# Performance work log

Hardware: AMD Instinct MI355X
Metric: run time of the kernel (lower is better)

## Reference

```python
import jax, jax.numpy as jnp
import numpy as np

BEAM = 8
MAX_LEN = 64
SOS_ID = 1
EOS_ID = 2
NEG = -1e30


def setup_inputs() -> dict:
    key = jax.random.key(0)
    ks = jax.random.split(key, 12)
    B, L, H, V, E = 16, 64, 1024, 32000, 1024
    s = 0.02
    return {
        "dec_hidden": jax.random.normal(ks[0], (B, H), jnp.float32),
        "q_enc_outputs": jax.random.normal(ks[1], (B, L, H), jnp.float32),
        "q_inputs_length": jax.random.randint(ks[2], (B,), 1, L + 1),
        "embedding": jax.random.normal(ks[3], (V, E), jnp.float32) * s,
        "W_ih": jax.random.normal(ks[4], (E, 3 * H), jnp.float32) * s,
        "W_hh": jax.random.normal(ks[5], (H, 3 * H), jnp.float32) * s,
        "b_ih": jnp.zeros((3 * H,), jnp.float32),
        "b_hh": jnp.zeros((3 * H,), jnp.float32),
        "W_c": jax.random.normal(ks[6], (2 * H, H), jnp.float32) * s,
        "W_out": jax.random.normal(ks[7], (H, V), jnp.float32) * s,
        "b_out": jnp.zeros((V,), jnp.float32),
    }


def _beam_search(dec_hidden, q_enc_outputs, q_inputs_length, embedding,
                 W_ih, W_hh, b_ih, b_hh, W_c, W_out, b_out):
    B, H = dec_hidden.shape
    L = q_enc_outputs.shape[1]
    V = W_out.shape[1]
    K = BEAM
    N = B * K
    pos_index = jnp.arange(B)[:, None] * K  # [B,1] offset of each batch's beam block

    # inflate encoder state beam_size times (beam is the inner dim: index = b*K + k)
    hidden = jnp.repeat(dec_hidden, K, axis=0)            # [N,H]
    q_enc = jnp.repeat(q_enc_outputs, K, axis=0)          # [N,L,H]
    q_len = jnp.repeat(q_inputs_length, K, axis=0)        # [N]
    len_mask = jnp.arange(L)[None, :] < q_len[:, None]    # [N,L]

    # only beam 0 of each batch starts live (score 0), rest -inf
    seq_scores = jnp.full((N,), NEG, jnp.float32).at[::K].set(0.0)
    dec_input = jnp.full((N,), SOS_ID, jnp.int32)

    def gru_cell(x, h):
        gx = x @ W_ih + b_ih
        gh = h @ W_hh + b_hh
        xr, xz, xn = jnp.split(gx, 3, axis=-1)
        hr, hz, hn = jnp.split(gh, 3, axis=-1)
        r = jax.nn.sigmoid(xr + hr)
        z = jax.nn.sigmoid(xz + hz)
        n = jnp.tanh(xn + r * hn)
        return (1.0 - z) * n + z * h

    def step(carry, _):
        hidden, seq_scores, dec_input = carry
        x = embedding[dec_input]                               # [N,E]
        h = gru_cell(x, hidden)                                # [N,H]
        # dot-product attention over encoder outputs
        att = jnp.einsum('nh,nlh->nl', h, q_enc) / jnp.sqrt(jnp.float32(H))
        att = jnp.where(len_mask, att, NEG)
        a = jax.nn.softmax(att, axis=-1)
        ctx = jnp.einsum('nl,nlh->nh', a, q_enc)
        o = jnp.tanh(jnp.concatenate([h, ctx], axis=-1) @ W_c)
        logits = o @ W_out + b_out                             # [N,V]
        logp = jax.nn.log_softmax(logits, axis=-1)
        # accumulate scores, flatten beams*vocab per batch, take top-K
        cand = (seq_scores[:, None] + logp).reshape(B, K * V)
        scores, idx = jax.lax.top_k(cand, K)                   # [B,K]
        symbols = (idx % V).reshape(N)
        preds = (idx // V + pos_index).reshape(N)              # predecessor beam rows
        new_hidden = h[preds]
        new_scores = scores.reshape(N)
        stored = new_scores                                     # stored before EOS mask
        new_scores = jnp.where(symbols == EOS_ID, NEG, new_scores)
        return (new_hidden, new_scores, symbols), (stored, preds, symbols)

    _, (all_scores, all_preds, all_syms) = jax.lax.scan(
        step, (hidden, seq_scores, dec_input), None, length=MAX_LEN)

    # backtrack: pick top-K final beams and trace predecessors backwards
    final_scores = all_scores[-1].reshape(B, K)
    sorted_score, sorted_idx = jax.lax.top_k(final_scores, K)
    t_pred = (sorted_idx + pos_index).reshape(N)

    def back(carry, xs):
        syms_t, preds_t = xs
        cur = syms_t[carry]
        return preds_t[carry], cur

    _, seq_rev = jax.lax.scan(back, t_pred, (all_syms[::-1], all_preds[::-1]))
    sequences = seq_rev[::-1].T.reshape(B, BEAM, MAX_LEN)
    return sorted_score, sequences


def reference(dec_hidden, q_enc_outputs, q_inputs_length, embedding,
              W_ih, W_hh, b_ih, b_hh, W_c, W_out, b_out):
    return _beam_search(dec_hidden, q_enc_outputs, q_inputs_length, embedding,
                        W_ih, W_hh, b_ih, b_hh, W_c, W_out, b_out)
```

## Files before the change

kernel.cpp:

```cpp
#include <hip/hip_runtime.h>
#include <cstdint>
#include <cstddef>
#include <climits>

#define Hdim 1024
#define Vdim 32000
#define Lq 64
#define Nrows 128
#define TMAX 64
#define NEGF (-1e30f)

__device__ __forceinline__ bool betterf(float av, int ai, float bv, int bi) {
  return (av > bv) || (av == bv && ai < bi);
}

__device__ __forceinline__ float tanh_xla(float x) {
  float ax = fabsf(x);
  float xc = fminf(fmaxf(x, -7.90531110763549805f), 7.90531110763549805f);
  float x2 = __fmul_rn(xc, xc);
  float p = -2.76076847742355e-16f;
  p = fmaf(p, x2, 2.00018790482477e-13f);
  p = fmaf(p, x2, -8.60467152213735e-11f);
  p = fmaf(p, x2, 5.12229709037114e-08f);
  p = fmaf(p, x2, 1.48572235717979e-05f);
  p = fmaf(p, x2, 6.37261928875436e-04f);
  p = fmaf(p, x2, 4.89352455891786e-03f);
  p = __fmul_rn(xc, p);
  float q = 1.19825839466702e-06f;
  q = fmaf(q, x2, 1.18534705686654e-04f);
  q = fmaf(q, x2, 2.26843463243900e-03f);
  q = fmaf(q, x2, 4.89352518554385e-03f);
  float r = __fdiv_rn(p, q);
  return (ax < 0.0004f) ? x : r;
}

__device__ __forceinline__ float sigmoid_xla(float x) {
  return __fadd_rn(0.5f, __fmul_rn(0.5f, tanh_xla(__fmul_rn(0.5f, x))));
}

__device__ __forceinline__ float exp_xla(float x) {
  x = fminf(x, 88.3762626647950f);
  x = fmaxf(x, -88.3762626647949f);
  float m = floorf(fmaf(x, 1.44269504088896341f, 0.5f));
  float r = fmaf(m, -0.693359375f, x);
  r = fmaf(m, 2.12194440e-4f, r);
  float r2 = __fmul_rn(r, r);
  float p = 1.9875691500e-4f;
  p = fmaf(p, r, 1.3981999507e-3f);
  p = fmaf(p, r, 8.3334519073e-3f);
  p = fmaf(p, r, 4.1665795894e-2f);
  p = fmaf(p, r, 1.6666665459e-1f);
  p = fmaf(p, r, 5.0000001201e-1f);
  p = fmaf(p, r2, r);
  p = __fadd_rn(p, 1.0f);
  int n = (int)m;
  float two_n = __int_as_float((n + 127) << 23);
  return __fmul_rn(p, two_n);
}

__device__ __forceinline__ float log_xla(float x) {
  int ix = __float_as_int(x);
  int e = ((ix >> 23) & 0xFF) - 126;
  float m = __int_as_float((ix & 0x007FFFFF) | 0x3F000000);
  if (m < 0.707106781186547524f) { e -= 1; m = __fadd_rn(m, m); }
  m = __fsub_rn(m, 1.0f);
  float z = __fmul_rn(m, m);
  float p = 7.0376836292e-2f;
  p = fmaf(p, m, -1.1514610310e-1f);
  p = fmaf(p, m, 1.1676998740e-1f);
  p = fmaf(p, m, -1.2420140846e-1f);
  p = fmaf(p, m, 1.4249322787e-1f);
  p = fmaf(p, m, -1.6668057665e-1f);
  p = fmaf(p, m, 2.0000714765e-1f);
  p = fmaf(p, m, -2.4999993993e-1f);
  p = fmaf(p, m, 3.3333331174e-1f);
  float ef = (float)e;
  float y = __fmul_rn(m, __fmul_rn(z, p));
  y = fmaf(ef, -2.12194440e-4f, y);
  y = fmaf(z, -0.5f, y);
  float res = __fadd_rn(m, y);
  res = fmaf(ef, 0.693359375f, res);
  return res;
}

template <int MT, int NT>
__device__ __forceinline__ void gemm_body(
    const float* __restrict__ A, int lda, const int* __restrict__ rowmap,
    const float* __restrict__ B, int ldb, const float* __restrict__ bias,
    float* __restrict__ C, int ldc, int K, int act, int n0, int m0)
{
  constexpr int RM = MT / 16, RN = NT / 16;
  __shared__ float As[32][MT + 1];
  __shared__ float Bs[32][NT + 1];
  __shared__ int rows[MT];
  const int t = threadIdx.x;
  if (t < MT) rows[t] = rowmap ? rowmap[m0 + t] : (m0 + t);
  __syncthreads();
  const int tm = t >> 4, tn = t & 15;
  float acc[RM][RN] = {};
  for (int kt = 0; kt < K; kt += 32) {
#pragma unroll
    for (int i = 0; i < MT / 8; ++i) {
      int idx = t + i * 256;
      int m = idx >> 5, kk = idx & 31;
      As[kk][m] = A[(size_t)rows[m] * lda + (size_t)(kt + kk)];
    }
#pragma unroll
    for (int i = 0; i < NT / 8; ++i) {
      int idx = t + i * 256;
      int kk = idx / NT, nn = idx % NT;
      Bs[kk][nn] = B[(size_t)(kt + kk) * ldb + (size_t)(n0 + nn)];
    }
    __syncthreads();
#pragma unroll
    for (int kk = 0; kk < 32; ++kk) {
      float a[RM], bb[RN];
#pragma unroll
      for (int i = 0; i < RM; ++i) a[i] = As[kk][tm * RM + i];
#pragma unroll
      for (int j = 0; j < RN; ++j) bb[j] = Bs[kk][tn * RN + j];
#pragma unroll
      for (int i = 0; i < RM; ++i)
#pragma unroll
        for (int j = 0; j < RN; ++j)
          acc[i][j] = fmaf(a[i], bb[j], acc[i][j]);
    }
    __syncthreads();
  }
#pragma unroll
  for (int i = 0; i < RM; ++i) {
    int m = m0 + tm * RM + i;
#pragma unroll
    for (int j = 0; j < RN; ++j) {
      int n = n0 + tn * RN + j;
      float v = acc[i][j];
      if (bias) v = __fadd_rn(v, bias[n]);
      if (act == 1) v = tanh_xla(v);
      C[(size_t)m * ldc + n] = v;
    }
  }
}

__global__ __launch_bounds__(256) void sgemm128(
    const float* __restrict__ A, int lda, const int* __restrict__ rowmap,
    const float* __restrict__ B, int ldb, const float* __restrict__ bias,
    float* __restrict__ C, int ldc, int K, int act)
{
  gemm_body<128, 64>(A, lda, rowmap, B, ldb, bias, C, ldc, K, act,
                     blockIdx.x * 64, 0);
}

__global__ __launch_bounds__(256) void gates_gemm(
    const float* __restrict__ emb, const int* __restrict__ symmap,
    const float* __restrict__ W_ih,
    const float* __restrict__ hprev, const int* __restrict__ hmap,
    const float* __restrict__ W_hh,
    float* __restrict__ gA, float* __restrict__ gB)
{
  if (blockIdx.z == 0)
    gemm_body<64, 64>(emb, 1024, symmap, W_ih, 3072, nullptr, gA, 3072, 1024, 0,
                      blockIdx.x * 64, blockIdx.y * 64);
  else
    gemm_body<64, 64>(hprev, 1024, hmap, W_hh, 3072, nullptr, gB, 3072, 1024, 0,
                      blockIdx.x * 64, blockIdx.y * 64);
}

__global__ __launch_bounds__(256) void sgemm_wc(
    const float* __restrict__ A2, const float* __restrict__ W_c,
    float* __restrict__ obuf)
{
  gemm_body<64, 32>(A2, 2048, nullptr, W_c, 1024, nullptr, obuf, 1024, 2048, 1,
                    blockIdx.x * 32, blockIdx.y * 64);
}

__global__ __launch_bounds__(256) void gru_gates(
    const float* __restrict__ gA, const float* __restrict__ gB,
    const float* __restrict__ b_ih, const float* __restrict__ b_hh,
    const float* __restrict__ hprev, const int* __restrict__ hmap,
    float* __restrict__ hout, float* __restrict__ A2)
{
  int n = blockIdx.x;
  int row = hmap[n];
  const float* hp = hprev + (size_t)row * Hdim;
  const float* a = gA + (size_t)n * 3 * Hdim;
  const float* g = gB + (size_t)n * 3 * Hdim;
  for (int j = threadIdx.x; j < Hdim; j += 256) {
    float xr = __fadd_rn(a[j],            b_ih[j]);
    float xz = __fadd_rn(a[Hdim + j],     b_ih[Hdim + j]);
    float xn = __fadd_rn(a[2 * Hdim + j], b_ih[2 * Hdim + j]);
    float hr = __fadd_rn(g[j],            b_hh[j]);
    float hz = __fadd_rn(g[Hdim + j],     b_hh[Hdim + j]);
    float hn = __fadd_rn(g[2 * Hdim + j], b_hh[2 * Hdim + j]);
    float r = sigmoid_xla(__fadd_rn(xr, hr));
    float z = sigmoid_xla(__fadd_rn(xz, hz));
    float t1 = __fmul_rn(r, hn);
    float nn = tanh_xla(__fadd_rn(xn, t1));
    float u1 = __fsub_rn(1.0f, z);
    float u2 = __fmul_rn(u1, nn);
    float u3 = __fmul_rn(z, hp[j]);
    float h = __fadd_rn(u2, u3);
    hout[(size_t)n * Hdim + j] = h;
    A2[(size_t)n * 2 * Hdim + j] = h;
  }
}

__global__ __launch_bounds__(256) void attn_kernel(
    const float* __restrict__ hnew, const float* __restrict__ q_enc,
    const int* __restrict__ q_len, float* __restrict__ A2)
{
  int n = blockIdx.x;
  int b = n >> 3;
  const float* q = q_enc + (size_t)b * Lq * Hdim;
  const float* hrow = hnew + (size_t)n * Hdim;
  __shared__ float att[Lq];
  __shared__ float ebuf[Lq];
  __shared__ float s_mx, s_sum;
  int t = threadIdx.x;
  if (t < Lq) {
    const float4* h4 = reinterpret_cast<const float4*>(hrow);
    const float4* q4 = reinterpret_cast<const float4*>(q + (size_t)t * Hdim);
    float acc[8];
#pragma unroll
    for (int j = 0; j < 8; ++j) acc[j] = 0.f;
    for (int i = 0; i < 128; ++i) {
      float4 ha = h4[2 * i], hb = h4[2 * i + 1];
      float4 qa = q4[2 * i], qb = q4[2 * i + 1];
      acc[0] = fmaf(ha.x, qa.x, acc[0]);
      acc[1] = fmaf(ha.y, qa.y, acc[1]);
      acc[2] = fmaf(ha.z, qa.z, acc[2]);
      acc[3] = fmaf(ha.w, qa.w, acc[3]);
      acc[4] = fmaf(hb.x, qb.x, acc[4]);
      acc[5] = fmaf(hb.y, qb.y, acc[5]);
      acc[6] = fmaf(hb.z, qb.z, acc[6]);
      acc[7] = fmaf(hb.w, qb.w, acc[7]);
    }
    float b0 = __fadd_rn(acc[0], acc[4]);
    float b1 = __fadd_rn(acc[1], acc[5]);
    float b2 = __fadd_rn(acc[2], acc[6]);
    float b3 = __fadd_rn(acc[3], acc[7]);
    float c0 = __fadd_rn(b0, b2);
    float c1 = __fadd_rn(b1, b3);
    float dot = __fadd_rn(c0, c1);
    att[t] = __fdiv_rn(dot, 32.0f);
  }
  __syncthreads();
  if (t == 0) {
    int len = q_len[b];
    float mx = -INFINITY;
    for (int l = 0; l < Lq; ++l) {
      float v = (l < len) ? att[l] : NEGF;
      att[l] = v;
      mx = fmaxf(mx, v);
    }
    s_mx = mx;
  }
  __syncthreads();
  if (t < Lq) ebuf[t] = exp_xla(__fsub_rn(att[t], s_mx));
  __syncthreads();
  if (t == 0) {
    float acc[8];
#pragma unroll
    for (int j = 0; j < 8; ++j) acc[j] = 0.f;
    for (int i = 0; i < 8; ++i) {
#pragma unroll
      for (int j = 0; j < 8; ++j) acc[j] = __fadd_rn(acc[j], ebuf[i * 8 + j]);
    }
    float b0 = __fadd_rn(acc[0], acc[4]);
    float b1 = __fadd_rn(acc[1], acc[5]);
    float b2 = __fadd_rn(acc[2], acc[6]);
    float b3 = __fadd_rn(acc[3], acc[7]);
    float c0 = __fadd_rn(b0, b2);
    float c1 = __fadd_rn(b1, b3);
    s_sum = __fadd_rn(c0, c1);
  }
  __syncthreads();
  if (t < Lq) att[t] = __fdiv_rn(ebuf[t], s_sum);
  __syncthreads();
#pragma unroll
  for (int hh = 0; hh < 4; ++hh) {
    int h = t + hh * 256;
    float c = 0.f;
    for (int l = 0; l < Lq; ++l) c = fmaf(att[l], q[(size_t)l * Hdim + h], c);
    A2[(size_t)n * 2 * Hdim + Hdim + h] = c;
  }
}

__global__ __launch_bounds__(256) void lse_kernel(const float* __restrict__ logits,
                                                  float* __restrict__ ebuf,
                                                  float* __restrict__ mxA,
                                                  float* __restrict__ lseA)
{
  int n = blockIdx.x;
  const float* row = logits + (size_t)n * Vdim;
  float* erow = ebuf + (size_t)n * Vdim;
  int t = threadIdx.x;
  int lane = t & 63, w = t >> 6;
  float mx = -INFINITY;
  for (int i = t; i < Vdim; i += 256) mx = fmaxf(mx, row[i]);
#pragma unroll
  for (int off = 32; off >= 1; off >>= 1) mx = fmaxf(mx, __shfl_xor(mx, off, 64));
  __shared__ float sm[4];
  __shared__ float lanes[8];
  if (lane == 0) sm[w] = mx;
  __syncthreads();
  mx = fmaxf(fmaxf(sm[0], sm[1]), fmaxf(sm[2], sm[3]));
  for (int i = t; i < Vdim; i += 256) erow[i] = exp_xla(__fsub_rn(row[i], mx));
  __syncthreads();
  if (t < 8) {
    float a = 0.f;
#pragma unroll 8
    for (int i = 0; i < 4000; ++i) a = __fadd_rn(a, erow[i * 8 + t]);
    lanes[t] = a;
  }
  __syncthreads();
  if (t == 0) {
    float b0 = __fadd_rn(lanes[0], lanes[4]);
    float b1 = __fadd_rn(lanes[1], lanes[5]);
    float b2 = __fadd_rn(lanes[2], lanes[6]);
    float b3 = __fadd_rn(lanes[3], lanes[7]);
    float c0 = __fadd_rn(b0, b2);
    float c1 = __fadd_rn(b1, b3);
    float s = __fadd_rn(c0, c1);
    mxA[n] = mx;
    lseA[n] = log_xla(s);
  }
}

__global__ __launch_bounds__(256) void topk_kernel(
    const float* __restrict__ logits, const float* __restrict__ mxA,
    const float* __restrict__ lseA, float* __restrict__ seq_scores,
    float* __restrict__ all_scores, int* __restrict__ all_preds,
    int* __restrict__ all_syms, int step)
{
  int b = blockIdx.x, t = threadIdx.x;
  __shared__ float s_seq[8], s_mx[8], s_lse[8];
  if (t < 8) {
    s_seq[t] = seq_scores[b * 8 + t];
    s_mx[t] = mxA[b * 8 + t];
    s_lse[t] = lseA[b * 8 + t];
  }
  __syncthreads();
  float lv[8]; int li[8];
#pragma unroll
  for (int r = 0; r < 8; ++r) { lv[r] = -INFINITY; li[r] = INT_MAX; }
  const float* base = logits + (size_t)b * 8 * Vdim;
  for (int c = t; c < 8 * Vdim; c += 256) {
    int k = c / Vdim;
    float sh = __fsub_rn(base[c], s_mx[k]);
    float lp = __fsub_rn(sh, s_lse[k]);
    float cand = __fadd_rn(s_seq[k], lp);
    if (betterf(cand, c, lv[7], li[7])) {
      lv[7] = cand; li[7] = c;
#pragma unroll
      for (int r = 7; r > 0; --r) {
        if (betterf(lv[r], li[r], lv[r - 1], li[r - 1])) {
          float tv = lv[r]; lv[r] = lv[r - 1]; lv[r - 1] = tv;
          int ti = li[r]; li[r] = li[r - 1]; li[r - 1] = ti;
        }
      }
    }
  }
  __shared__ float sv[256][8];
  __shared__ int si[256][8];
#pragma unroll
  for (int r = 0; r < 8; ++r) { sv[t][r] = lv[r]; si[t][r] = li[r]; }
  __syncthreads();
  if (t == 0) {
    for (int u = 1; u < 256; ++u) {
#pragma unroll
      for (int r = 0; r < 8; ++r) {
        float v = sv[u][r]; int ix = si[u][r];
        if (betterf(v, ix, lv[7], li[7])) {
          lv[7] = v; li[7] = ix;
#pragma unroll
          for (int q = 7; q > 0; --q) {
            if (betterf(lv[q], li[q], lv[q - 1], li[q - 1])) {
              float tv = lv[q]; lv[q] = lv[q - 1]; lv[q - 1] = tv;
              int ti = li[q]; li[q] = li[q - 1]; li[q - 1] = ti;
            }
          }
        } else break;
      }
    }
#pragma unroll
    for (int r = 0; r < 8; ++r) {
      int idx = li[r];
      int sym = idx % Vdim;
      int pred = idx / Vdim + b * 8;
      int n = b * 8 + r;
      all_scores[step * Nrows + n] = lv[r];
      all_preds[step * Nrows + n] = pred;
      all_syms[step * Nrows + n] = sym;
      seq_scores[n] = (sym == 2) ? NEGF : lv[r];
    }
  }
}

__global__ void init_kernel(float* seq_scores, int* init_hmap, int* init_sym) {
  int t = threadIdx.x;
  if (t < 128) {
    seq_scores[t] = ((t & 7) == 0) ? 0.0f : NEGF;
    init_hmap[t] = t >> 3;
    init_sym[t] = 1;
  }
}

__global__ void final_topk(const float* __restrict__ all_scores,
                           int* __restrict__ tpred, float* __restrict__ out_scores) {
  int b = threadIdx.x;
  if (b >= 16) return;
  float v[8]; int ki[8];
#pragma unroll
  for (int k = 0; k < 8; ++k) { v[k] = all_scores[63 * Nrows + b * 8 + k]; ki[k] = k; }
#pragma unroll
  for (int p = 0; p < 7; ++p)
#pragma unroll
    for (int i = 0; i < 7; ++i) {
      if (!betterf(v[i], ki[i], v[i + 1], ki[i + 1])) {
        float tv = v[i]; v[i] = v[i + 1]; v[i + 1] = tv;
        int ti = ki[i]; ki[i] = ki[i + 1]; ki[i + 1] = ti;
      }
    }
#pragma unroll
  for (int j = 0; j < 8; ++j) {
    out_scores[b * 8 + j] = v[j];
    tpred[b * 8 + j] = b * 8 + ki[j];
  }
}

__global__ void backtrack(const int* __restrict__ all_syms, const int* __restrict__ all_preds,
                          const int* __restrict__ tpred, float* __restrict__ out_seq) {
  int n = threadIdx.x;
  if (n >= 128) return;
  int carry = tpred[n];
  for (int tt = 63; tt >= 0; --tt) {
    int sym = all_syms[tt * Nrows + carry];
    out_seq[(size_t)n * 64 + tt] = (float)sym;
    carry = all_preds[tt * Nrows + carry];
  }
}

extern "C" void kernel_launch(void* const* d_in, const int* in_sizes, int n_in,
                              void* d_out, int out_size, void* d_ws, size_t ws_size,
                              hipStream_t stream) {
  (void)in_sizes; (void)n_in; (void)out_size; (void)ws_size;
  const float* dec_hidden = (const float*)d_in[0];
  const float* q_enc      = (const float*)d_in[1];
  const int*   q_len      = (const int*)d_in[2];
  const float* embedding  = (const float*)d_in[3];
  const float* W_ih       = (const float*)d_in[4];
  const float* W_hh       = (const float*)d_in[5];
  const float* b_ih       = (const float*)d_in[6];
  const float* b_hh       = (const float*)d_in[7];
  const float* W_c        = (const float*)d_in[8];
  const float* W_out      = (const float*)d_in[9];
  const float* b_out      = (const float*)d_in[10];
  float* out_scores = (float*)d_out;
  float* out_seq    = (float*)d_out + 128;

  char* w = (char*)d_ws;
  auto alloc = [&](size_t bytes) {
    char* p = w;
    w += (bytes + 255) & ~(size_t)255;
    return p;
  };
  float* hbuf0 = (float*)alloc((size_t)128 * 1024 * 4);
  float* hbuf1 = (float*)alloc((size_t)128 * 1024 * 4);
  float* A2    = (float*)alloc((size_t)128 * 2048 * 4);
  float* obuf  = (float*)alloc((size_t)128 * 1024 * 4);
  float* gA    = (float*)alloc((size_t)128 * 3072 * 4);
  float* gB    = (float*)alloc((size_t)128 * 3072 * 4);
  float* logits = (float*)alloc((size_t)128 * 32000 * 4);
  float* ebuf   = (float*)alloc((size_t)128 * 32000 * 4);
  float* mxA   = (float*)alloc(128 * 4);
  float* lseA  = (float*)alloc(128 * 4);
  float* seq_scores = (float*)alloc(128 * 4);
  int* init_hmap = (int*)alloc(128 * 4);
  int* init_sym  = (int*)alloc(128 * 4);
  int* tpred     = (int*)alloc(128 * 4);
  float* all_scores = (float*)alloc((size_t)64 * 128 * 4);
  int* all_preds = (int*)alloc((size_t)64 * 128 * 4);
  int* all_syms  = (int*)alloc((size_t)64 * 128 * 4);

  init_kernel<<<1, 128, 0, stream>>>(seq_scores, init_hmap, init_sym);

  for (int t = 0; t < TMAX; ++t) {
    const int* symmap = (t == 0) ? init_sym : (all_syms + (t - 1) * Nrows);
    const int* hmap   = (t == 0) ? init_hmap : (all_preds + (t - 1) * Nrows);
    const float* hprev = (t == 0) ? dec_hidden : (((t - 1) & 1) ? hbuf1 : hbuf0);
    float* hcur = (t & 1) ? hbuf1 : hbuf0;

    gates_gemm<<<dim3(48, 2, 2), 256, 0, stream>>>(
        embedding, symmap, W_ih, hprev, hmap, W_hh, gA, gB);
    gru_gates<<<128, 256, 0, stream>>>(gA, gB, b_ih, b_hh, hprev, hmap, hcur, A2);
    attn_kernel<<<128, 256, 0, stream>>>(hcur, q_enc, q_len, A2);
    sgemm_wc<<<dim3(32, 2), 256, 0, stream>>>(A2, W_c, obuf);
    sgemm128<<<500, 256, 0, stream>>>(obuf, 1024, nullptr, W_out, 32000,
                                      b_out, logits, 32000, 1024, 0);
    lse_kernel<<<128, 256, 0, stream>>>(logits, ebuf, mxA, lseA);
    topk_kernel<<<16, 256, 0, stream>>>(logits, mxA, lseA, seq_scores,
                                        all_scores, all_preds, all_syms, t);
  }

  final_topk<<<1, 128, 0, stream>>>(all_scores, tpred, out_scores);
  backtrack<<<1, 128, 0, stream>>>(all_syms, all_preds, tpred, out_seq);
}
```

Baseline: 73.56 ms.

## Vectorize GEMM tile loads with float4 and retile all GEMMs

The shared GEMM body now loads A and B tiles with float4 global reads and reads fragments from shared memory with float2/float4 loads, using padding of 4 to keep alignment. The logits GEMM moves to a 128x128 tile with 250 blocks. The gates and W_c GEMMs use smaller M tiles so more blocks are launched. The lse and topk kernels also read logits as float4. The aim is fewer memory instructions and better parallelism, at the cost of possible LDS bank conflicts from the transposed A stores and higher register pressure in the 128x128 tile.

```diff
diff --git a/kernel.cpp b/kernel.cpp
--- a/kernel.cpp
+++ b/kernel.cpp
@@ -90,8 +90,9 @@
     float* __restrict__ C, int ldc, int K, int act, int n0, int m0)
 {
   constexpr int RM = MT / 16, RN = NT / 16;
-  __shared__ float As[32][MT + 1];
-  __shared__ float Bs[32][NT + 1];
+  constexpr int PA = MT + 4, PB = NT + 4;
+  __shared__ float As[32][PA];
+  __shared__ float Bs[32][PB];
   __shared__ int rows[MT];
   const int t = threadIdx.x;
   if (t < MT) rows[t] = rowmap ? rowmap[m0 + t] : (m0 + t);
@@ -100,25 +101,50 @@
   float acc[RM][RN] = {};
   for (int kt = 0; kt < K; kt += 32) {
 #pragma unroll
-    for (int i = 0; i < MT / 8; ++i) {
+    for (int i = 0; i < MT / 32; ++i) {
       int idx = t + i * 256;
-      int m = idx >> 5, kk = idx & 31;
-      As[kk][m] = A[(size_t)rows[m] * lda + (size_t)(kt + kk)];
-    }
-#pragma unroll
-    for (int i = 0; i < NT / 8; ++i) {
+      int m = idx >> 3, k4 = idx & 7;
+      float4 v = *reinterpret_cast<const float4*>(
+          &A[(size_t)rows[m] * lda + (size_t)(kt + k4 * 4)]);
+      As[k4 * 4 + 0][m] = v.x;
+      As[k4 * 4 + 1][m] = v.y;
+      As[k4 * 4 + 2][m] = v.z;
+      As[k4 * 4 + 3][m] = v.w;
+    }
+#pragma unroll
+    for (int i = 0; i < NT / 32; ++i) {
       int idx = t + i * 256;
-      int kk = idx / NT, nn = idx % NT;
-      Bs[kk][nn] = B[(size_t)(kt + kk) * ldb + (size_t)(n0 + nn)];
+      int kk = idx / (NT / 4), n4 = idx % (NT / 4);
+      float4 v = *reinterpret_cast<const float4*>(
+          &B[(size_t)(kt + kk) * ldb + (size_t)(n0 + n4 * 4)]);
+      *reinterpret_cast<float4*>(&Bs[kk][n4 * 4]) = v;
     }
     __syncthreads();
 #pragma unroll
     for (int kk = 0; kk < 32; ++kk) {
       float a[RM], bb[RN];
-#pragma unroll
-      for (int i = 0; i < RM; ++i) a[i] = As[kk][tm * RM + i];
-#pragma unroll
-      for (int j = 0; j < RN; ++j) bb[j] = Bs[kk][tn * RN + j];
+      if constexpr (RM == 2) {
+        float2 v = *reinterpret_cast<const float2*>(&As[kk][tm * 2]);
+        a[0] = v.x; a[1] = v.y;
+      } else {
+#pragma unroll
+        for (int c = 0; c < RM / 4; ++c) {
+          float4 v = *reinterpret_cast<const float4*>(&As[kk][tm * RM + c * 4]);
+          a[c * 4 + 0] = v.x; a[c * 4 + 1] = v.y;
+          a[c * 4 + 2] = v.z; a[c * 4 + 3] = v.w;
+        }
+      }
+      if constexpr (RN == 2) {
+        float2 v = *reinterpret_cast<const float2*>(&Bs[kk][tn * 2]);
+        bb[0] = v.x; bb[1] = v.y;
+      } else {
+#pragma unroll
+        for (int c = 0; c < RN / 4; ++c) {
+          float4 v = *reinterpret_cast<const float4*>(&Bs[kk][tn * RN + c * 4]);
+          bb[c * 4 + 0] = v.x; bb[c * 4 + 1] = v.y;
+          bb[c * 4 + 2] = v.z; bb[c * 4 + 3] = v.w;
+        }
+      }
 #pragma unroll
       for (int i = 0; i < RM; ++i)
 #pragma unroll
@@ -141,13 +167,12 @@
   }
 }
 
-__global__ __launch_bounds__(256) void sgemm128(
-    const float* __restrict__ A, int lda, const int* __restrict__ rowmap,
-    const float* __restrict__ B, int ldb, const float* __restrict__ bias,
-    float* __restrict__ C, int ldc, int K, int act)
-{
-  gemm_body<128, 64>(A, lda, rowmap, B, ldb, bias, C, ldc, K, act,
-                     blockIdx.x * 64, 0);
+__global__ __launch_bounds__(256) void sgemm_logits(
+    const float* __restrict__ A, const float* __restrict__ B,
+    const float* __restrict__ bias, float* __restrict__ C)
+{
+  gemm_body<128, 128>(A, 1024, nullptr, B, 32000, bias, C, 32000, 1024, 0,
+                      blockIdx.x * 128, 0);
 }
 
 __global__ __launch_bounds__(256) void gates_gemm(
@@ -158,19 +183,19 @@
     float* __restrict__ gA, float* __restrict__ gB)
 {
   if (blockIdx.z == 0)
-    gemm_body<64, 64>(emb, 1024, symmap, W_ih, 3072, nullptr, gA, 3072, 1024, 0,
-                      blockIdx.x * 64, blockIdx.y * 64);
+    gemm_body<32, 64>(emb, 1024, symmap, W_ih, 3072, nullptr, gA, 3072, 1024, 0,
+                      blockIdx.x * 64, blockIdx.y * 32);
   else
-    gemm_body<64, 64>(hprev, 1024, hmap, W_hh, 3072, nullptr, gB, 3072, 1024, 0,
-                      blockIdx.x * 64, blockIdx.y * 64);
+    gemm_body<32, 64>(hprev, 1024, hmap, W_hh, 3072, nullptr, gB, 3072, 1024, 0,
+                      blockIdx.x * 64, blockIdx.y * 32);
 }
 
 __global__ __launch_bounds__(256) void sgemm_wc(
     const float* __restrict__ A2, const float* __restrict__ W_c,
     float* __restrict__ obuf)
 {
-  gemm_body<64, 32>(A2, 2048, nullptr, W_c, 1024, nullptr, obuf, 1024, 2048, 1,
-                    blockIdx.x * 32, blockIdx.y * 64);
+  gemm_body<32, 32>(A2, 2048, nullptr, W_c, 1024, nullptr, obuf, 1024, 2048, 1,
+                    blockIdx.x * 32, blockIdx.y * 32);
 }
 
 __global__ __launch_bounds__(256) void gru_gates(
@@ -295,8 +320,13 @@
   float* erow = ebuf + (size_t)n * Vdim;
   int t = threadIdx.x;
   int lane = t & 63, w = t >> 6;
+  const float4* row4 = reinterpret_cast<const float4*>(row);
+  float4* erow4 = reinterpret_cast<float4*>(erow);
   float mx = -INFINITY;
-  for (int i = t; i < Vdim; i += 256) mx = fmaxf(mx, row[i]);
+  for (int i = t; i < 8000; i += 256) {
+    float4 v = row4[i];
+    mx = fmaxf(mx, fmaxf(fmaxf(v.x, v.y), fmaxf(v.z, v.w)));
+  }
 #pragma unroll
   for (int off = 32; off >= 1; off >>= 1) mx = fmaxf(mx, __shfl_xor(mx, off, 64));
   __shared__ float sm[4];
@@ -304,7 +334,15 @@
   if (lane == 0) sm[w] = mx;
   __syncthreads();
   mx = fmaxf(fmaxf(sm[0], sm[1]), fmaxf(sm[2], sm[3]));
-  for (int i = t; i < Vdim; i += 256) erow[i] = exp_xla(__fsub_rn(row[i], mx));
+  for (int i = t; i < 8000; i += 256) {
+    float4 v = row4[i];
+    float4 e;
+    e.x = exp_xla(__fsub_rn(v.x, mx));
+    e.y = exp_xla(__fsub_rn(v.y, mx));
+    e.z = exp_xla(__fsub_rn(v.z, mx));
+    e.w = exp_xla(__fsub_rn(v.w, mx));
+    erow4[i] = e;
+  }
   __syncthreads();
   if (t < 8) {
     float a = 0.f;
@@ -343,19 +381,26 @@
   float lv[8]; int li[8];
 #pragma unroll
   for (int r = 0; r < 8; ++r) { lv[r] = -INFINITY; li[r] = INT_MAX; }
-  const float* base = logits + (size_t)b * 8 * Vdim;
-  for (int c = t; c < 8 * Vdim; c += 256) {
-    int k = c / Vdim;
-    float sh = __fsub_rn(base[c], s_mx[k]);
-    float lp = __fsub_rn(sh, s_lse[k]);
-    float cand = __fadd_rn(s_seq[k], lp);
-    if (betterf(cand, c, lv[7], li[7])) {
-      lv[7] = cand; li[7] = c;
-#pragma unroll
-      for (int r = 7; r > 0; --r) {
-        if (betterf(lv[r], li[r], lv[r - 1], li[r - 1])) {
-          float tv = lv[r]; lv[r] = lv[r - 1]; lv[r - 1] = tv;
-          int ti = li[r]; li[r] = li[r - 1]; li[r - 1] = ti;
+  const float4* base4 = reinterpret_cast<const float4*>(logits + (size_t)b * 8 * Vdim);
+  for (int c4 = t; c4 < 64000; c4 += 256) {
+    float4 v4 = base4[c4];
+    int cb = c4 * 4;
+#pragma unroll
+    for (int e = 0; e < 4; ++e) {
+      int c = cb + e;
+      int k = c / Vdim;
+      float x = (e == 0) ? v4.x : (e == 1) ? v4.y : (e == 2) ? v4.z : v4.w;
+      float sh = __fsub_rn(x, s_mx[k]);
+      float lp = __fsub_rn(sh, s_lse[k]);
+      float cand = __fadd_rn(s_seq[k], lp);
+      if (betterf(cand, c, lv[7], li[7])) {
+        lv[7] = cand; li[7] = c;
+#pragma unroll
+        for (int r = 7; r > 0; --r) {
+          if (betterf(lv[r], li[r], lv[r - 1], li[r - 1])) {
+            float tv = lv[r]; lv[r] = lv[r - 1]; lv[r - 1] = tv;
+            int ti = li[r]; li[r] = li[r - 1]; li[r - 1] = ti;
+          }
         }
       }
     }
@@ -490,13 +535,12 @@
     const float* hprev = (t == 0) ? dec_hidden : (((t - 1) & 1) ? hbuf1 : hbuf0);
     float* hcur = (t & 1) ? hbuf1 : hbuf0;
 
-    gates_gemm<<<dim3(48, 2, 2), 256, 0, stream>>>(
+    gates_gemm<<<dim3(48, 4, 2), 256, 0, stream>>>(
         embedding, symmap, W_ih, hprev, hmap, W_hh, gA, gB);
     gru_gates<<<128, 256, 0, stream>>>(gA, gB, b_ih, b_hh, hprev, hmap, hcur, A2);
     attn_kernel<<<128, 256, 0, stream>>>(hcur, q_enc, q_len, A2);
-    sgemm_wc<<<dim3(32, 2), 256, 0, stream>>>(A2, W_c, obuf);
-    sgemm128<<<500, 256, 0, stream>>>(obuf, 1024, nullptr, W_out, 32000,
-                                      b_out, logits, 32000, 1024, 0);
+    sgemm_wc<<<dim3(32, 4), 256, 0, stream>>>(A2, W_c, obuf);
+    sgemm_logits<<<250, 256, 0, stream>>>(obuf, W_out, b_out, logits);
     lse_kernel<<<128, 256, 0, stream>>>(logits, ebuf, mxA, lseA);
     topk_kernel<<<16, 256, 0, stream>>>(logits, mxA, lseA, seq_scores,
                                         all_scores, all_preds, all_syms, t);
```

After: 63.29 ms. 1.16x faster.
